# Kernel tuning notes

Hardware: AMD Instinct MI355X
Metric: run time of the kernel (lower is better)

The kernel has to match this reference:

```python
import jax, jax.numpy as jnp
import numpy as np


def setup_inputs() -> dict:
    key = jax.random.key(0)
    k1, k2, k3 = jax.random.split(key, 3)
    N, C_in, H, W = 32, 16, 256, 256
    C_out, K = 64, 3
    x = jax.random.normal(k1, (N, C_in, H, W), dtype=jnp.float32)
    # match nn.Conv2d default init scale roughly (values irrelevant for correctness harness)
    fan_in = C_in * K * K
    bound = 1.0 / np.sqrt(fan_in)
    conv_weight = jax.random.normal(k2, (C_out, C_in, K, K), dtype=jnp.float32) * bound
    conv_bias = jax.random.normal(k3, (C_out,), dtype=jnp.float32) * bound
    return {"x": x, "conv_weight": conv_weight, "conv_bias": conv_bias}


def reference(x, conv_weight, conv_bias):
    # Conv2d: stride=1, padding=0 (VALID), dilation=1, groups=1
    y = jax.lax.conv_general_dilated(
        x, conv_weight,
        window_strides=(1, 1), padding='VALID',
        dimension_numbers=('NCHW', 'OIHW', 'NCHW'),
    ) + conv_bias[None, :, None, None]          # (N, C_out, OH, OW)
    y = jnp.min(y, axis=1, keepdims=True)       # min over output channels -> (N, 1, OH, OW)
    return jnp.tanh(jnp.tanh(y))                # double tanh
```

## Files before the change

### kernel.cpp

```cpp
#include <hip/hip_runtime.h>
#include <hip/hip_bf16.h>

typedef __attribute__((ext_vector_type(8)))  short short8;
typedef __attribute__((ext_vector_type(4)))  float f32x4;
typedef __attribute__((ext_vector_type(16))) float f32x16;

#define CIN   16
#define HH    256
#define WW    256
#define OHH   254
#define OWW   254

#define HSTR   (36 * 8)
#define HALF   (34 * HSTR + 8)

__device__ __forceinline__ ushort f2bf(float f) {
    unsigned u = __builtin_bit_cast(unsigned, f);
    unsigned r = (u + 0x7fffu + ((u >> 16) & 1u)) >> 16;
    return (ushort)r;
}

__device__ __forceinline__ float dtanh2(float x) {
    const float K = 2.8853900817779268f;
    float xc = fminf(fmaxf(x, -9.0f), 9.0f);
    float e1 = __builtin_amdgcn_exp2f(K * xc);
    float t1 = 1.0f - 2.0f * __builtin_amdgcn_rcpf(e1 + 1.0f);
    float e2 = __builtin_amdgcn_exp2f(K * t1);
    return 1.0f - 2.0f * __builtin_amdgcn_rcpf(e2 + 1.0f);
}

__global__ void prep_weights(const float* __restrict__ wsrc, ushort* __restrict__ wfrag) {
    int idx = blockIdx.x * 256 + threadIdx.x;
    if (idx >= 9216) return;
    int r    = idx & 7;
    int lane = (idx >> 3) & 63;
    int j    = (idx >> 9) & 1;
    int tap  = idx >> 10;
    int ci   = 8 * (lane >> 5) + r;
    int co   = j * 32 + (lane & 31);
    int kh   = tap / 3, kw = tap - 3 * kh;
    wfrag[idx] = f2bf(wsrc[(co * CIN + ci) * 9 + kh * 3 + kw]);
}

__global__ __launch_bounds__(256, 3) void conv_min_tanh(
        const float* __restrict__ x, const ushort* __restrict__ wfrag,
        const float* __restrict__ bias, float* __restrict__ out) {
    __shared__ ushort lds[2 * HALF];
    __shared__ ushort mp[2][32][32];

    const int tid = threadIdx.x;
    const int n   = blockIdx.z;
    const int oh0 = blockIdx.y * 32;
    const int ow0 = blockIdx.x * 32;
    const int HW  = HH * WW;
    const float* xb = x + (size_t)n * CIN * HW;

    auto stage0 = [&](int pos) {
        int hp  = pos / 36;
        int r2  = pos - hp * 36;
        int ciq = r2 / 9;
        int w4  = r2 - ciq * 9;
        int hg  = min(oh0 + hp, HH - 1);
        int wg  = min(ow0 + 4 * w4, WW - 4);
        const float* src = xb + (size_t)(ciq * 4) * HW + hg * WW + wg;
        f32x4 v0 = *reinterpret_cast<const f32x4*>(src);
        f32x4 v1 = *reinterpret_cast<const f32x4*>(src + HW);
        f32x4 v2 = *reinterpret_cast<const f32x4*>(src + 2 * HW);
        f32x4 v3 = *reinterpret_cast<const f32x4*>(src + 3 * HW);
        ushort* dst = &lds[(ciq >> 1) * HALF + (hp * 36 + 4 * w4) * 8 + (ciq & 1) * 4];
#pragma unroll
        for (int e = 0; e < 4; ++e) {
            unsigned lo, hi;
            asm("v_cvt_pk_bf16_f32 %0, %1, %2" : "=v"(lo) : "v"(v0[e]), "v"(v1[e]));
            asm("v_cvt_pk_bf16_f32 %0, %1, %2" : "=v"(hi) : "v"(v2[e]), "v"(v3[e]));
            uint2 pk; pk.x = lo; pk.y = hi;
            *reinterpret_cast<uint2*>(dst + e * 8) = pk;
        }
    };
    stage0(tid);
    if (tid < 104) stage0(tid + 256);

    const int lr0  = tid / 36;
    const int rm0  = tid - lr0 * 36;
    const int ciq0 = rm0 / 9;
    const int w40  = rm0 - ciq0 * 9;
    const int wg0  = min(ow0 + 4 * w40, WW - 4);
    const int gc0  = ciq0 * 4 * HW + wg0;
    const bool two = (tid < 32);
    const int ciq1 = (4 + tid) / 9;
    const int w41  = (4 + tid) - ciq1 * 9;
    const int wg1  = min(ow0 + 4 * w41, WW - 4);
    const int gc1  = ciq1 * 4 * HW + wg1;
    const int ld0  = (ciq0 >> 1) * HALF + (4 * w40) * 8 + (ciq0 & 1) * 4;
    const int ld1  = (ciq1 >> 1) * HALF + (4 * w41) * 8 + (ciq1 & 1) * 4;

    const int lane  = tid & 63;
    const int wid   = tid >> 6;
    const int jw    = wid & 1;
    const int rq    = wid >> 1;
    const int px    = lane & 31;
    const int khalf = lane >> 5;

    short8 wf[9];
#pragma unroll
    for (int tap = 0; tap < 9; ++tap)
        wf[tap] = *reinterpret_cast<const short8*>(wfrag + ((tap * 2 + jw) * 64 + lane) * 8);
    f32x16 bi;
#pragma unroll
    for (int q4 = 0; q4 < 4; ++q4) {
        f32x4 b = *reinterpret_cast<const f32x4*>(bias + jw * 32 + 4 * khalf + 8 * q4);
#pragma unroll
        for (int s = 0; s < 4; ++s) bi[q4 * 4 + s] = b[s];
    }
    const ushort* bptr = &lds[khalf * HALF + (rq * 4) * HSTR + px * 8];

    __syncthreads();

    f32x4 ra0, ra1, ra2, ra3, rb0, rb1, rb2, rb3;

#pragma unroll
    for (int q = 0; q < 4; ++q) {
        if (q < 3) {
            const int c = q + 1;
            {
                int hg = min(oh0 + 8 * c + 2 + lr0, HH - 1);
                const float* s = xb + gc0 + hg * WW;
                asm volatile("global_load_dwordx4 %0, %1, off" : "=v"(ra0) : "v"(s) : "memory");
                asm volatile("global_load_dwordx4 %0, %1, off" : "=v"(ra1) : "v"(s + HW) : "memory");
                asm volatile("global_load_dwordx4 %0, %1, off" : "=v"(ra2) : "v"(s + 2 * HW) : "memory");
                asm volatile("global_load_dwordx4 %0, %1, off" : "=v"(ra3) : "v"(s + 3 * HW) : "memory");
            }
            if (two) {
                int hg = min(oh0 + 8 * c + 2 + 7, HH - 1);
                const float* s = xb + gc1 + hg * WW;
                asm volatile("global_load_dwordx4 %0, %1, off" : "=v"(rb0) : "v"(s) : "memory");
                asm volatile("global_load_dwordx4 %0, %1, off" : "=v"(rb1) : "v"(s + HW) : "memory");
                asm volatile("global_load_dwordx4 %0, %1, off" : "=v"(rb2) : "v"(s + 2 * HW) : "memory");
                asm volatile("global_load_dwordx4 %0, %1, off" : "=v"(rb3) : "v"(s + 3 * HW) : "memory");
            }
        }

#pragma unroll
        for (int i = 0; i < 4; ++i) {
            f32x16 a = bi;
#pragma unroll
            for (int kh = 0; kh < 3; ++kh)
#pragma unroll
                for (int kw = 0; kw < 3; ++kw) {
                    short8 b = *reinterpret_cast<const short8*>(
                        bptr + (8 * q + i + kh) * HSTR + kw * 8);
                    a = __builtin_amdgcn_mfma_f32_32x32x16_bf16(wf[kh * 3 + kw], b, a, 0, 0, 0);
                }
            float v = a[0];
#pragma unroll
            for (int r = 1; r < 16; ++r) v = fminf(v, a[r]);
            v = fminf(v, __shfl_xor(v, 32, 64));
            if (lane < 32) mp[jw][8 * q + rq * 4 + i][px] = f2bf(v);
        }

        if (q < 3) {
            asm volatile("s_waitcnt vmcnt(0)" ::: "memory");
            const int c = q + 1;
            {
                ushort* dst = &lds[ld0 + ((8 * c + 2 + lr0) * 36) * 8];
#pragma unroll
                for (int e = 0; e < 4; ++e) {
                    unsigned lo, hi;
                    asm("v_cvt_pk_bf16_f32 %0, %1, %2" : "=v"(lo) : "v"(ra0[e]), "v"(ra1[e]));
                    asm("v_cvt_pk_bf16_f32 %0, %1, %2" : "=v"(hi) : "v"(ra2[e]), "v"(ra3[e]));
                    uint2 pk; pk.x = lo; pk.y = hi;
                    *reinterpret_cast<uint2*>(dst + e * 8) = pk;
                }
            }
            if (two) {
                ushort* dst = &lds[ld1 + ((8 * c + 2 + 7) * 36) * 8];
#pragma unroll
                for (int e = 0; e < 4; ++e) {
                    unsigned lo, hi;
                    asm("v_cvt_pk_bf16_f32 %0, %1, %2" : "=v"(lo) : "v"(rb0[e]), "v"(rb1[e]));
                    asm("v_cvt_pk_bf16_f32 %0, %1, %2" : "=v"(hi) : "v"(rb2[e]), "v"(rb3[e]));
                    uint2 pk; pk.x = lo; pk.y = hi;
                    *reinterpret_cast<uint2*>(dst + e * 8) = pk;
                }
            }
            __syncthreads();
        }
    }

    __syncthreads();

    const int row = tid >> 3, px4 = (tid & 7) * 4;
    uint2 p0 = *reinterpret_cast<const uint2*>(&mp[0][row][px4]);
    uint2 p1 = *reinterpret_cast<const uint2*>(&mp[1][row][px4]);
    f32x4 y;
#pragma unroll
    for (int e = 0; e < 4; ++e) {
        unsigned w0 = (e < 2) ? p0.x : p0.y;
        unsigned w1 = (e < 2) ? p1.x : p1.y;
        float f0 = __builtin_bit_cast(float, (e & 1) ? (w0 & 0xffff0000u) : (w0 << 16));
        float f1 = __builtin_bit_cast(float, (e & 1) ? (w1 & 0xffff0000u) : (w1 << 16));
        y[e] = dtanh2(fminf(f0, f1));
    }
    const int oh = oh0 + row, ow = ow0 + px4;
    if (oh < OHH) {
        float* op = &out[((size_t)n * OHH + oh) * OWW + ow];
        if (ow + 3 < OWW) {
            *reinterpret_cast<f32x4*>(op) = y;
        } else {
#pragma unroll
            for (int e = 0; e < 4; ++e)
                if (ow + e < OWW) op[e] = y[e];
        }
    }
}

extern "C" void kernel_launch(void* const* d_in, const int* in_sizes, int n_in,
                              void* d_out, int out_size, void* d_ws, size_t ws_size,
                              hipStream_t stream) {
    const float* x = (const float*)d_in[0];
    const float* w = (const float*)d_in[1];
    const float* b = (const float*)d_in[2];
    float* out     = (float*)d_out;
    ushort* wfrag  = (ushort*)d_ws;

    prep_weights<<<36, 256, 0, stream>>>(w, wfrag);
    dim3 grid(8, 8, 32);
    conv_min_tanh<<<grid, dim3(256, 1, 1), 0, stream>>>(x, wfrag, b, out);
}
```

Before: 55.15 us.

## Rebalance prologue staging and reuse LDS row fragments across output rows

The prologue now stages 16 input rows instead of 10, so each later pipeline stage loads only 6 new rows and is handled by a single load set per thread. The old second load set (rb) for 32 threads goes away. The MFMA inner loop keeps a sliding window of three rows of B fragments in registers, so each output row reads one new row (3 fragments) from LDS instead of 9. The costs are a longer unpipelined prologue and more live VGPRs for the window, which could affect occupancy at launch_bounds(256,3).

```diff
diff --git a/kernel.cpp b/kernel.cpp
--- a/kernel.cpp
+++ b/kernel.cpp
@@ -78,21 +78,17 @@
         }
     };
     stage0(tid);
-    if (tid < 104) stage0(tid + 256);
-
-    const int lr0  = tid / 36;
-    const int rm0  = tid - lr0 * 36;
-    const int ciq0 = rm0 / 9;
-    const int w40  = rm0 - ciq0 * 9;
-    const int wg0  = min(ow0 + 4 * w40, WW - 4);
-    const int gc0  = ciq0 * 4 * HW + wg0;
-    const bool two = (tid < 32);
-    const int ciq1 = (4 + tid) / 9;
-    const int w41  = (4 + tid) - ciq1 * 9;
-    const int wg1  = min(ow0 + 4 * w41, WW - 4);
-    const int gc1  = ciq1 * 4 * HW + wg1;
-    const int ld0  = (ciq0 >> 1) * HALF + (4 * w40) * 8 + (ciq0 & 1) * 4;
-    const int ld1  = (ciq1 >> 1) * HALF + (4 * w41) * 8 + (ciq1 & 1) * 4;
+    stage0(tid + 256);
+    if (tid < 64) stage0(tid + 512);
+
+    const bool sa   = (tid < 216);
+    const int lr0   = tid / 36;
+    const int rm0   = tid - lr0 * 36;
+    const int ciq0  = rm0 / 9;
+    const int w40   = rm0 - ciq0 * 9;
+    const int wg0   = min(ow0 + 4 * w40, WW - 4);
+    const int gc0   = ciq0 * 4 * HW + wg0;
+    const int ld0   = (ciq0 >> 1) * HALF + (4 * w40) * 8 + (ciq0 & 1) * 4;
 
     const int lane  = tid & 63;
     const int wid   = tid >> 6;
@@ -116,53 +112,57 @@
 
     __syncthreads();
 
-    f32x4 ra0, ra1, ra2, ra3, rb0, rb1, rb2, rb3;
+    f32x4 ra0, ra1, ra2, ra3;
 
 #pragma unroll
     for (int q = 0; q < 4; ++q) {
-        if (q < 3) {
-            const int c = q + 1;
-            {
-                int hg = min(oh0 + 8 * c + 2 + lr0, HH - 1);
-                const float* s = xb + gc0 + hg * WW;
-                asm volatile("global_load_dwordx4 %0, %1, off" : "=v"(ra0) : "v"(s) : "memory");
-                asm volatile("global_load_dwordx4 %0, %1, off" : "=v"(ra1) : "v"(s + HW) : "memory");
-                asm volatile("global_load_dwordx4 %0, %1, off" : "=v"(ra2) : "v"(s + 2 * HW) : "memory");
-                asm volatile("global_load_dwordx4 %0, %1, off" : "=v"(ra3) : "v"(s + 3 * HW) : "memory");
+        if (q < 3 && sa) {
+            int hg = min(oh0 + 16 + 6 * q + lr0, HH - 1);
+            const float* s = xb + gc0 + hg * WW;
+            asm volatile("global_load_dwordx4 %0, %1, off" : "=v"(ra0) : "v"(s) : "memory");
+            asm volatile("global_load_dwordx4 %0, %1, off" : "=v"(ra1) : "v"(s + HW) : "memory");
+            asm volatile("global_load_dwordx4 %0, %1, off" : "=v"(ra2) : "v"(s + 2 * HW) : "memory");
+            asm volatile("global_load_dwordx4 %0, %1, off" : "=v"(ra3) : "v"(s + 3 * HW) : "memory");
+        }
+
+        {
+            const int base = 8 * q;
+            short8 w0[3], w1[3];
+#pragma unroll
+            for (int kw = 0; kw < 3; ++kw) {
+                w0[kw] = *reinterpret_cast<const short8*>(bptr + (base + 0) * HSTR + kw * 8);
+                w1[kw] = *reinterpret_cast<const short8*>(bptr + (base + 1) * HSTR + kw * 8);
             }
-            if (two) {
-                int hg = min(oh0 + 8 * c + 2 + 7, HH - 1);
-                const float* s = xb + gc1 + hg * WW;
-                asm volatile("global_load_dwordx4 %0, %1, off" : "=v"(rb0) : "v"(s) : "memory");
-                asm volatile("global_load_dwordx4 %0, %1, off" : "=v"(rb1) : "v"(s + HW) : "memory");
-                asm volatile("global_load_dwordx4 %0, %1, off" : "=v"(rb2) : "v"(s + 2 * HW) : "memory");
-                asm volatile("global_load_dwordx4 %0, %1, off" : "=v"(rb3) : "v"(s + 3 * HW) : "memory");
+#pragma unroll
+            for (int i = 0; i < 4; ++i) {
+                short8 fr[3];
+#pragma unroll
+                for (int kw = 0; kw < 3; ++kw)
+                    fr[kw] = *reinterpret_cast<const short8*>(bptr + (base + i + 2) * HSTR + kw * 8);
+                f32x16 a = bi;
+#pragma unroll
+                for (int kw = 0; kw < 3; ++kw)
+                    a = __builtin_amdgcn_mfma_f32_32x32x16_bf16(wf[kw], w0[kw], a, 0, 0, 0);
+#pragma unroll
+                for (int kw = 0; kw < 3; ++kw)
+                    a = __builtin_amdgcn_mfma_f32_32x32x16_bf16(wf[3 + kw], w1[kw], a, 0, 0, 0);
+#pragma unroll
+                for (int kw = 0; kw < 3; ++kw)
+                    a = __builtin_amdgcn_mfma_f32_32x32x16_bf16(wf[6 + kw], fr[kw], a, 0, 0, 0);
+                float v = a[0];
+#pragma unroll
+                for (int r = 1; r < 16; ++r) v = fminf(v, a[r]);
+                v = fminf(v, __shfl_xor(v, 32, 64));
+                if (lane < 32) mp[jw][8 * q + rq * 4 + i][px] = f2bf(v);
+#pragma unroll
+                for (int kw = 0; kw < 3; ++kw) { w0[kw] = w1[kw]; w1[kw] = fr[kw]; }
             }
-        }
-
-#pragma unroll
-        for (int i = 0; i < 4; ++i) {
-            f32x16 a = bi;
-#pragma unroll
-            for (int kh = 0; kh < 3; ++kh)
-#pragma unroll
-                for (int kw = 0; kw < 3; ++kw) {
-                    short8 b = *reinterpret_cast<const short8*>(
-                        bptr + (8 * q + i + kh) * HSTR + kw * 8);
-                    a = __builtin_amdgcn_mfma_f32_32x32x16_bf16(wf[kh * 3 + kw], b, a, 0, 0, 0);
-                }
-            float v = a[0];
-#pragma unroll
-            for (int r = 1; r < 16; ++r) v = fminf(v, a[r]);
-            v = fminf(v, __shfl_xor(v, 32, 64));
-            if (lane < 32) mp[jw][8 * q + rq * 4 + i][px] = f2bf(v);
         }
 
         if (q < 3) {
             asm volatile("s_waitcnt vmcnt(0)" ::: "memory");
-            const int c = q + 1;
-            {
-                ushort* dst = &lds[ld0 + ((8 * c + 2 + lr0) * 36) * 8];
+            if (sa) {
+                ushort* dst = &lds[ld0 + ((16 + 6 * q + lr0) * 36) * 8];
 #pragma unroll
                 for (int e = 0; e < 4; ++e) {
                     unsigned lo, hi;
@@ -172,17 +172,6 @@
                     *reinterpret_cast<uint2*>(dst + e * 8) = pk;
                 }
             }
-            if (two) {
-                ushort* dst = &lds[ld1 + ((8 * c + 2 + 7) * 36) * 8];
-#pragma unroll
-                for (int e = 0; e < 4; ++e) {
-                    unsigned lo, hi;
-                    asm("v_cvt_pk_bf16_f32 %0, %1, %2" : "=v"(lo) : "v"(rb0[e]), "v"(rb1[e]));
-                    asm("v_cvt_pk_bf16_f32 %0, %1, %2" : "=v"(hi) : "v"(rb2[e]), "v"(rb3[e]));
-                    uint2 pk; pk.x = lo; pk.y = hi;
-                    *reinterpret_cast<uint2*>(dst + e * 8) = pk;
-                }
-            }
             __syncthreads();
         }
     }
```

Result: slower. 56.52 us (+2.5%).
